# Performance work log

Hardware: AMD Instinct MI355X
Metric: run time of the kernel (lower is better)

Reference implementation:

```python
import jax, jax.numpy as jnp
import numpy as np

B, K, C, D, L, H, FF = 64, 1024, 512, 256, 2, 4, 1024
DH = D // H
EPS = 1e-5
NEG = -jnp.inf
SCALE = 1.0 / float(np.sqrt(DH))


def _ln(x, w, b):
    m = x.mean(-1, keepdims=True)
    v = ((x - m) ** 2).mean(-1, keepdims=True)
    return (x - m) * jax.lax.rsqrt(v + EPS) * w + b


def _star_attn(x, key_pad, pad_c, Wq, bq, Wk, bk, Wv, bv, Wo, bo):
    # Star topology: rows 0,1 (query,dustbin) attend to all non-padded keys;
    # each candidate row attends only to {query, dustbin, itself}.
    Bb, S, _ = x.shape
    q = (x @ Wq.T + bq).reshape(Bb, S, H, DH)
    k = (x @ Wk.T + bk).reshape(Bb, S, H, DH)
    v = (x @ Wv.T + bv).reshape(Bb, S, H, DH)
    # global rows
    qg = q[:, :2]
    sg = jnp.einsum('bthd,bshd->bhts', qg, k) * SCALE            # [B,H,2,S]
    sg = jnp.where(key_pad[:, None, None, :], NEG, sg)
    out_g = jnp.einsum('bhts,bshd->bthd', jax.nn.softmax(sg, -1), v)  # [B,2,H,DH]
    # candidate rows: scores against the 2 global keys + self key
    qc, kc, vc = q[:, 2:], k[:, 2:], v[:, 2:]
    kg, vg = k[:, :2], v[:, :2]
    s2 = jnp.einsum('bkhd,bthd->bkht', qc, kg) * SCALE           # [B,K,H,2]
    ss = jnp.einsum('bkhd,bkhd->bkh', qc, kc) * SCALE            # [B,K,H]
    ss = jnp.where(pad_c[:, :, None], NEG, ss)                   # padded self-key disallowed
    w = jax.nn.softmax(jnp.concatenate([s2, ss[..., None]], -1), -1)  # [B,K,H,3]
    out_c = jnp.einsum('bkht,bthd->bkhd', w[..., :2], vg) + w[..., 2:] * vc
    out = jnp.concatenate([out_g, out_c], 1).reshape(Bb, S, D)
    return out @ Wo.T + bo


def _forward(query, candidates, candidate_mask, qp_w, qp_b, cp_w, cp_b,
             dustbin, type_emb, ln1_w, ln1_b, ln2_w, ln2_b,
             Wq, bq, Wk, bk, Wv, bv, Wo, bo,
             ff1_w, ff1_b, ff2_w, ff2_b, head_ln_w, head_ln_b, head_w, head_b):
    Bb = query.shape[0]
    qt = (query @ qp_w.T + qp_b + type_emb[0])[:, None]          # [B,1,D]
    dt = jnp.broadcast_to(dustbin + type_emb[1], (Bb, 1, D))
    ct = candidates @ cp_w.T + cp_b + type_emb[2]                # [B,K,D]
    x = jnp.concatenate([qt, dt, ct], 1)                         # [B,K+2,D]
    pad_c = jnp.logical_not(candidate_mask)
    key_pad = jnp.concatenate([jnp.zeros((Bb, 2), bool), pad_c], 1)
    for l in range(L):  # pre-LN encoder layers (norm_first, eval so dropout=0)
        x = x + _star_attn(_ln(x, ln1_w[l], ln1_b[l]), key_pad, pad_c,
                           Wq[l], bq[l], Wk[l], bk[l], Wv[l], bv[l], Wo[l], bo[l])
        h = _ln(x, ln2_w[l], ln2_b[l])
        x = x + (jax.nn.gelu(h @ ff1_w[l].T + ff1_b[l], approximate=False) @ ff2_w[l].T + ff2_b[l])
    logits = (_ln(x, head_ln_w, head_ln_b) @ head_w.T + head_b)[..., 0]  # [B,K+2]
    cand = jnp.where(candidate_mask, logits[:, 2:], NEG)
    return jnp.concatenate([logits[:, 1:2], cand], 1)            # [B,K+1]


def setup_inputs() -> dict:
    key = jax.random.key(0)
    ks = iter(jax.random.split(key, 40))
    n = lambda shape, s=0.02: jax.random.normal(next(ks), shape, jnp.float32) * s
    return dict(
        query=jax.random.normal(next(ks), (B, C), jnp.float32),
        candidates=jax.random.normal(next(ks), (B, K, C), jnp.float32),
        candidate_mask=jax.random.bernoulli(next(ks), 0.9, (B, K)),
        qp_w=n((D, C)), qp_b=jnp.zeros(D),
        cp_w=n((D, C)), cp_b=jnp.zeros(D),
        dustbin=n((D,)), type_emb=n((3, D)),
        ln1_w=jnp.ones((L, D)), ln1_b=jnp.zeros((L, D)),
        ln2_w=jnp.ones((L, D)), ln2_b=jnp.zeros((L, D)),
        Wq=n((L, D, D)), bq=jnp.zeros((L, D)),
        Wk=n((L, D, D)), bk=jnp.zeros((L, D)),
        Wv=n((L, D, D)), bv=jnp.zeros((L, D)),
        Wo=n((L, D, D)), bo=jnp.zeros((L, D)),
        ff1_w=n((L, FF, D)), ff1_b=jnp.zeros((L, FF)),
        ff2_w=n((L, D, FF)), ff2_b=jnp.zeros((L, D)),
        head_ln_w=jnp.ones(D), head_ln_b=jnp.zeros(D),
        head_w=n((1, D)), head_b=jnp.zeros(1),
    )


def reference(query, candidates, candidate_mask, qp_w, qp_b, cp_w, cp_b,
              dustbin, type_emb, ln1_w, ln1_b, ln2_w, ln2_b,
              Wq, bq, Wk, bk, Wv, bv, Wo, bo,
              ff1_w, ff1_b, ff2_w, ff2_b, head_ln_w, head_ln_b, head_w, head_b):
    return _forward(query, candidates, candidate_mask, qp_w, qp_b, cp_w, cp_b,
                    dustbin, type_emb, ln1_w, ln1_b, ln2_w, ln2_b,
                    Wq, bq, Wk, bk, Wv, bv, Wo, bo,
                    ff1_w, ff1_b, ff2_w, ff2_b, head_ln_w, head_ln_b, head_w, head_b)
```

## Files before the change

kernel.cpp:

```cpp
#include <hip/hip_runtime.h>
#include <math.h>

static constexpr int Bc = 64;
static constexpr int Kc = 1024;
static constexpr int Cc = 512;
static constexpr int Dc = 256;
static constexpr int Hc = 4;
static constexpr int Sc = 1026;
static constexpr int FFc = 1024;
static constexpr float EPSc = 1e-5f;
static constexpr float SCALEc = 0.125f;
static constexpr float NEG_OUT = -1.0e30f;

typedef __attribute__((ext_vector_type(8))) short short8;
typedef __attribute__((ext_vector_type(8))) unsigned short u16x8;
typedef __attribute__((ext_vector_type(4))) float f32x4;

__device__ __forceinline__ float bf2f(unsigned short u) {
  union { float f; unsigned int i; } c; c.i = ((unsigned int)u) << 16; return c.f;
}
__device__ __forceinline__ unsigned short f2bf(float f) {
  union { float f; unsigned int i; } c; c.f = f;
  unsigned int i = c.i;
  unsigned int r = (i + 0x7fffu + ((i >> 16) & 1u)) >> 16;
  return (unsigned short)r;
}
__device__ __forceinline__ unsigned int cvt_pk_bf16(float a, float b) {
  unsigned int d;
  asm("v_cvt_pk_bf16_f32 %0, %1, %2" : "=v"(d) : "v"(a), "v"(b));
  return d;
}

__device__ __forceinline__ float wave_sum(float v) {
#pragma unroll
  for (int off = 32; off > 0; off >>= 1) v += __shfl_xor(v, off, 64);
  return v;
}
__device__ __forceinline__ float wave_max(float v) {
#pragma unroll
  for (int off = 32; off > 0; off >>= 1) v = fmaxf(v, __shfl_xor(v, off, 64));
  return v;
}

__device__ __forceinline__ void async_ld16(const unsigned short* g, unsigned short* l) {
  __builtin_amdgcn_global_load_lds(
      (const __attribute__((address_space(1))) void*)g,
      (__attribute__((address_space(3))) void*)l, 16, 0, 0);
}

__device__ __forceinline__ float gelu_fast(float u) {
  const float z = u * fmaf(u * u, 0.07135481627f, 1.5957691216f);
  return __fdividef(u, 1.0f + __expf(-z));
}

template <int EPI, int MAP, int CASTA>
__global__ __launch_bounds__(256) void gemm_mfma(
    const void* __restrict__ Av, const unsigned short* __restrict__ W,
    const float* __restrict__ bias, const void* extra,
    void* Cout, int N, int Kd, int ldc, int MB, int NB) {
  __shared__ unsigned short lds[24576];
  const int xcd = blockIdx.x & 7;
  const int slot = blockIdx.x >> 3;
  const int nb = slot % NB;
  const int mb = (slot / NB) * 8 + xcd;
  if (mb >= MB) return;
  const int m0 = mb * 128;
  const int n0 = nb * 128;
  const int tid = threadIdx.x;
  const int w = tid >> 6;
  const int lane = tid & 63;

  const unsigned short* A = (const unsigned short*)Av;
  const float* Af = (const float*)Av;

  const int srA[2] = {(w * 2 + 0) * 16 + (lane >> 2), (w * 2 + 1) * 16 + (lane >> 2)};
  const unsigned short* pA[2];
  const unsigned short* pB[2];
#pragma unroll
  for (int c = 0; c < 2; ++c) {
    const int kc = ((lane & 3) ^ ((srA[c] >> 1) & 3)) * 8;
    if (!CASTA) pA[c] = A + (size_t)(m0 + srA[c]) * Kd + kc;
    pB[c] = W + (size_t)(n0 + srA[c]) * Kd + kc;
  }
  const int lreg0 = (w * 2 + 0) * 512;
  const int lreg1 = (w * 2 + 1) * 512;

  f32x4 zero = {0.f, 0.f, 0.f, 0.f};
  f32x4 acc[4][4];
#pragma unroll
  for (int i = 0; i < 4; ++i)
#pragma unroll
    for (int j = 0; j < 4; ++j) acc[i][j] = zero;

  const int mrow = (w & 1) * 64;
  const int nrow = (w >> 1) * 64;
  const int l15 = lane & 15;
  const int quad = lane >> 4;
  const int koff = (quad ^ ((l15 >> 1) & 3)) * 16;

  auto stage = [&](int kk, int b) {
    if (CASTA) {
#pragma unroll
      for (int wi = 0; wi < 4; ++wi) {
        const int g = wi * 256 + tid;
        const int row = g >> 3;
        const int k4 = g & 7;
        const int phys =
            row * 32 + ((((k4 >> 1) ^ ((row >> 1) & 3))) << 3) + ((k4 & 1) << 2);
        const float4 a4 =
            *(const float4*)(Af + (size_t)(m0 + row) * Kd + kk + k4 * 4);
        uint2 o;
        o.x = cvt_pk_bf16(a4.x, a4.y);
        o.y = cvt_pk_bf16(a4.z, a4.w);
        *(uint2*)(&lds[b * 4096 + phys]) = o;
      }
    } else {
      async_ld16(pA[0] + kk, &lds[b * 4096 + lreg0]);
      async_ld16(pA[1] + kk, &lds[b * 4096 + lreg1]);
    }
    async_ld16(pB[0] + kk, &lds[12288 + b * 4096 + lreg0]);
    async_ld16(pB[1] + kk, &lds[12288 + b * 4096 + lreg1]);
  };

  auto compute_tile = [&](int cur) {
    const char* AsB = (const char*)&lds[cur * 4096];
    const char* WsB = (const char*)&lds[12288 + cur * 4096];
    short8 af[4], bfr[4];
#pragma unroll
    for (int i = 0; i < 4; ++i)
      af[i] = *(const short8*)(AsB + (size_t)(mrow + i * 16 + l15) * 64 + koff);
#pragma unroll
    for (int j = 0; j < 4; ++j)
      bfr[j] = *(const short8*)(WsB + (size_t)(nrow + j * 16 + l15) * 64 + koff);
#pragma unroll
    for (int i = 0; i < 4; ++i)
#pragma unroll
      for (int j = 0; j < 4; ++j)
        acc[i][j] = __builtin_amdgcn_mfma_f32_16x16x32_bf16(bfr[j], af[i],
                                                            acc[i][j], 0, 0, 0);
  };

  const int niter = Kd >> 5;
  if (CASTA) {
    stage(0, 0);
    for (int it = 0; it < niter; ++it) {
      const int cur = it & 1;
      __syncthreads();
      if (it + 1 < niter) stage((it + 1) << 5, cur ^ 1);
      compute_tile(cur);
    }
  } else {
    stage(0, 0);
    stage(32, 1);
    int cur = 0;
    for (int it = 0; it < niter; ++it) {
      if (it + 1 < niter)
        asm volatile("s_waitcnt vmcnt(4)" ::: "memory");
      else
        asm volatile("s_waitcnt vmcnt(0)" ::: "memory");
      asm volatile("s_waitcnt lgkmcnt(0)" ::: "memory");
      __builtin_amdgcn_s_barrier();
      if (it + 2 < niter) {
        int b2 = cur + 2; if (b2 >= 3) b2 -= 3;
        stage((it + 2) << 5, b2);
      }
      compute_tile(cur);
      cur = (cur == 2) ? 0 : cur + 1;
    }
  }

  const float* extraF = (const float*)extra;
  const unsigned short* extraB = (const unsigned short*)extra;
  float4 bj[4];
#pragma unroll
  for (int j = 0; j < 4; ++j) {
    const int n = n0 + nrow + j * 16 + quad * 4;
    float4 t4 = *(const float4*)(bias + n);
    if (EPI == 1) {
      const float4 e4 = *(const float4*)(extraF + n);
      t4.x += e4.x; t4.y += e4.y; t4.z += e4.z; t4.w += e4.w;
    }
    bj[j] = t4;
  }
  __syncthreads();
#pragma unroll
  for (int i = 0; i < 4; ++i) {
    const int m = mrow + i * 16 + l15;
    const int swz = (m & 7) << 1;
#pragma unroll
    for (int j = 0; j < 4; ++j) {
      float v0 = acc[i][j][0] + bj[j].x;
      float v1 = acc[i][j][1] + bj[j].y;
      float v2 = acc[i][j][2] + bj[j].z;
      float v3 = acc[i][j][3] + bj[j].w;
      if (EPI == 3) {
        v0 = gelu_fast(v0); v1 = gelu_fast(v1);
        v2 = gelu_fast(v2); v3 = gelu_fast(v3);
      }
      uint2 pk;
      pk.x = cvt_pk_bf16(v0, v1);
      pk.y = cvt_pk_bf16(v2, v3);
      const int g = ((nrow + j * 16 + quad * 4) >> 2) ^ swz;
      *(uint2*)(&lds[m * 128 + g * 4]) = pk;
    }
  }
  __syncthreads();
  unsigned short* outb = (unsigned short*)Cout;
#pragma unroll
  for (int c8 = 0; c8 < 8; ++c8) {
    const int idx = c8 * 256 + tid;
    const int row = idx >> 4;
    const int cc = idx & 15;
    const int gsr = (2 * cc) ^ ((row & 7) << 1);
    u16x8 val = *(const u16x8*)(&lds[row * 128 + gsr * 4]);
    const int col = cc * 8;
    const int m = m0 + row;
    const size_t orow =
        (MAP == 1) ? ((size_t)(m >> 10) * Sc + 2 + (m & 1023)) : (size_t)m;
    const size_t go = orow * (size_t)ldc + n0 + col;
    if (EPI == 2) {
      u16x8 rv = *(const u16x8*)(extraB + go);
      unsigned int* vp = (unsigned int*)&val;
#pragma unroll
      for (int e = 0; e < 4; ++e) {
        const float a0 = bf2f(val[2 * e]) + bf2f(rv[2 * e]);
        const float a1 = bf2f(val[2 * e + 1]) + bf2f(rv[2 * e + 1]);
        vp[e] = cvt_pk_bf16(a0, a1);
      }
    }
    *(u16x8*)(outb + go) = val;
  }
}

struct CastTab {
  const float* src[10];
  unsigned short* dst[10];
  int n4[10];
};
__global__ __launch_bounds__(256) void cast_multi(CastTab t) {
  const int e = blockIdx.y;
  const int n4 = t.n4[e];
  const float4* s = (const float4*)t.src[e];
  uint2* d = (uint2*)t.dst[e];
  for (int i = blockIdx.x * 256 + threadIdx.x; i < n4; i += gridDim.x * 256) {
    float4 f = s[i];
    uint2 o;
    o.x = cvt_pk_bf16(f.x, f.y);
    o.y = cvt_pk_bf16(f.z, f.w);
    d[i] = o;
  }
}

__global__ __launch_bounds__(256) void bias_concat(const float* bq, const float* bk,
                                                   const float* bv, float* qkvb) {
  const int i = blockIdx.x * 256 + threadIdx.x;
  if (i >= 2 * 768) return;
  const int l = i / 768;
  const int j = i - l * 768;
  float v;
  if (j < 256) v = bq[l * 256 + j];
  else if (j < 512) v = bk[l * 256 + j - 256];
  else v = bv[l * 256 + j - 512];
  qkvb[i] = v;
}

__global__ __launch_bounds__(256) void embed_qd(
    const float* __restrict__ qin, const float* __restrict__ qp_w,
    const float* __restrict__ qp_b, const float* __restrict__ dustbin,
    const float* __restrict__ type_emb, unsigned short* __restrict__ x) {
  const int b = blockIdx.x;
  const int d = threadIdx.x;
  __shared__ __align__(16) float qs[512];
  qs[d] = qin[b * 512 + d];
  qs[d + 256] = qin[b * 512 + 256 + d];
  __syncthreads();
  float acc = 0.0f;
  const float* wr = qp_w + (size_t)d * 512;
#pragma unroll 4
  for (int c = 0; c < 512; c += 4) {
    float4 w4 = *(const float4*)(wr + c);
    acc = fmaf(qs[c], w4.x, acc);
    acc = fmaf(qs[c + 1], w4.y, acc);
    acc = fmaf(qs[c + 2], w4.z, acc);
    acc = fmaf(qs[c + 3], w4.w, acc);
  }
  const size_t base = (size_t)b * Sc * Dc;
  x[base + d] = f2bf(acc + qp_b[d] + type_emb[d]);
  x[base + Dc + d] = f2bf(dustbin[d] + type_emb[Dc + d]);
}

__global__ __launch_bounds__(256) void ln_kernel(
    const unsigned short* __restrict__ x, const float* __restrict__ w,
    const float* __restrict__ b, unsigned short* __restrict__ y, int nrows) {
  const int wave = threadIdx.x >> 6;
  const int lane = threadIdx.x & 63;
  const int row = blockIdx.x * 4 + wave;
  if (row >= nrows) return;
  const unsigned short* xr = x + (size_t)row * Dc;
  ushort4 xv = *(const ushort4*)(xr + lane * 4);
  const float v0 = bf2f(xv.x), v1 = bf2f(xv.y), v2 = bf2f(xv.z), v3 = bf2f(xv.w);
  float s = v0 + v1 + v2 + v3;
  float sq = v0 * v0 + v1 * v1 + v2 * v2 + v3 * v3;
  s = wave_sum(s);
  sq = wave_sum(sq);
  const float mean = s * (1.0f / Dc);
  const float var = sq * (1.0f / Dc) - mean * mean;
  const float rs = rsqrtf(var + EPSc);
  float4 wv = *(const float4*)(w + lane * 4);
  float4 bv = *(const float4*)(b + lane * 4);
  uint2 o;
  o.x = cvt_pk_bf16((v0 - mean) * rs * wv.x + bv.x,
                    (v1 - mean) * rs * wv.y + bv.y);
  o.y = cvt_pk_bf16((v2 - mean) * rs * wv.z + bv.z,
                    (v3 - mean) * rs * wv.w + bv.w);
  *(uint2*)(y + (size_t)row * Dc + lane * 4) = o;
}

__global__ __launch_bounds__(256) void attn_global(
    const unsigned short* __restrict__ qkv, const unsigned char* __restrict__ mask,
    unsigned short* __restrict__ ao) {
  const int b = blockIdx.x;
  const int h = blockIdx.y;
  const int tid = threadIdx.x;
  const int wv = tid >> 6;
  const int lane = tid & 63;
  __shared__ float q0s[64], q1s[64];
  __shared__ float sc0[Sc], sc1[Sc];
  __shared__ float rbuf[4][2];
  __shared__ float obuf[2][4][64];
  const size_t base = (size_t)b * Sc * 768 + h * 64;
  if (tid < 64) {
    q0s[tid] = bf2f(qkv[base + tid]);
    q1s[tid] = bf2f(qkv[base + 768 + tid]);
  }
  __syncthreads();

  float lm0 = -INFINITY, lm1 = -INFINITY;
  for (int s = tid; s < Sc; s += 256) {
    const unsigned short* kr = qkv + base + 256 + (size_t)s * 768;
    float d0 = 0.0f, d1 = 0.0f;
#pragma unroll
    for (int c = 0; c < 64; c += 8) {
      u16x8 kv = *(const u16x8*)(kr + c);
#pragma unroll
      for (int e = 0; e < 8; ++e) {
        const float kf = bf2f(kv[e]);
        d0 = fmaf(q0s[c + e], kf, d0);
        d1 = fmaf(q1s[c + e], kf, d1);
      }
    }
    const bool pad = (s >= 2) && (mask[b * Kc + (s - 2)] == 0);
    const float s0 = pad ? -INFINITY : d0 * SCALEc;
    const float s1 = pad ? -INFINITY : d1 * SCALEc;
    sc0[s] = s0; sc1[s] = s1;
    lm0 = fmaxf(lm0, s0); lm1 = fmaxf(lm1, s1);
  }
  lm0 = wave_max(lm0);
  lm1 = wave_max(lm1);
  if (lane == 0) { rbuf[wv][0] = lm0; rbuf[wv][1] = lm1; }
  __syncthreads();
  const float m0 = fmaxf(fmaxf(rbuf[0][0], rbuf[1][0]), fmaxf(rbuf[2][0], rbuf[3][0]));
  const float m1 = fmaxf(fmaxf(rbuf[0][1], rbuf[1][1]), fmaxf(rbuf[2][1], rbuf[3][1]));
  float ls0 = 0.0f, ls1 = 0.0f;
  for (int s = tid; s < Sc; s += 256) {
    const float e0 = expf(sc0[s] - m0);
    const float e1 = expf(sc1[s] - m1);
    sc0[s] = e0; sc1[s] = e1;
    ls0 += e0; ls1 += e1;
  }
  ls0 = wave_sum(ls0);
  ls1 = wave_sum(ls1);
  __syncthreads();
  if (lane == 0) { rbuf[wv][0] = ls0; rbuf[wv][1] = ls1; }
  __syncthreads();
  const float t0 = rbuf[0][0] + rbuf[1][0] + rbuf[2][0] + rbuf[3][0];
  const float t1 = rbuf[0][1] + rbuf[1][1] + rbuf[2][1] + rbuf[3][1];
  float o0 = 0.0f, o1 = 0.0f;
  for (int s = wv; s < Sc; s += 4) {
    const float vvv = bf2f(qkv[base + 512 + (size_t)s * 768 + lane]);
    o0 = fmaf(sc0[s], vvv, o0);
    o1 = fmaf(sc1[s], vvv, o1);
  }
  obuf[0][wv][lane] = o0;
  obuf[1][wv][lane] = o1;
  __syncthreads();
  if (wv == 0) {
    const float a0 = obuf[0][0][lane] + obuf[0][1][lane] + obuf[0][2][lane] + obuf[0][3][lane];
    const float a1 = obuf[1][0][lane] + obuf[1][1][lane] + obuf[1][2][lane] + obuf[1][3][lane];
    const size_t ob = ((size_t)b * Sc) * Dc + h * 64;
    ao[ob + lane] = f2bf(a0 / t0);
    ao[ob + Dc + lane] = f2bf(a1 / t1);
  }
}

__global__ __launch_bounds__(256) void attn_cand(
    const unsigned short* __restrict__ qkv, const unsigned char* __restrict__ mask,
    unsigned short* __restrict__ ao) {
  const int bk = blockIdx.x;
  const int b = bk >> 10;
  const int kk = bk & 1023;
  const int h = threadIdx.x >> 6;
  const int lane = threadIdx.x & 63;
  const size_t rowg = (size_t)b * Sc * 768 + h * 64;
  const size_t rowc = rowg + (size_t)(2 + kk) * 768;
  const float qc = bf2f(qkv[rowc + lane]);
  float p0 = qc * bf2f(qkv[rowg + 256 + lane]);
  float p1 = qc * bf2f(qkv[rowg + 256 + 768 + lane]);
  float p2 = qc * bf2f(qkv[rowc + 256 + lane]);
#pragma unroll
  for (int off = 32; off > 0; off >>= 1) {
    p0 += __shfl_xor(p0, off, 64);
    p1 += __shfl_xor(p1, off, 64);
    p2 += __shfl_xor(p2, off, 64);
  }
  const bool pad = (mask[b * Kc + kk] == 0);
  const float s0 = p0 * SCALEc;
  const float s1 = p1 * SCALEc;
  const float s2 = pad ? -INFINITY : p2 * SCALEc;
  const float m = fmaxf(fmaxf(s0, s1), s2);
  const float e0 = expf(s0 - m);
  const float e1 = expf(s1 - m);
  const float e2 = pad ? 0.0f : expf(s2 - m);
  const float inv = 1.0f / (e0 + e1 + e2);
  const float o = (e0 * bf2f(qkv[rowg + 512 + lane]) +
                   e1 * bf2f(qkv[rowg + 512 + 768 + lane]) +
                   e2 * bf2f(qkv[rowc + 512 + lane])) * inv;
  ao[((size_t)b * Sc + 2 + kk) * Dc + h * 64 + lane] = f2bf(o);
}

__global__ __launch_bounds__(256) void head_kernel(
    const unsigned short* __restrict__ x, const float* __restrict__ lnw,
    const float* __restrict__ lnb, const float* __restrict__ hw,
    const float* __restrict__ hb, const unsigned char* __restrict__ mask,
    float* __restrict__ out) {
  const int gw = blockIdx.x * 4 + (threadIdx.x >> 6);
  const int lane = threadIdx.x & 63;
  if (gw >= Bc * 1025) return;
  const int b = gw / 1025;
  const int j = gw - b * 1025;
  const int s = 1 + j;
  const unsigned short* xr = x + ((size_t)b * Sc + s) * Dc;
  ushort4 xv = *(const ushort4*)(xr + lane * 4);
  const float v0 = bf2f(xv.x), v1 = bf2f(xv.y), v2 = bf2f(xv.z), v3 = bf2f(xv.w);
  float su = v0 + v1 + v2 + v3;
  float sq = v0 * v0 + v1 * v1 + v2 * v2 + v3 * v3;
  su = wave_sum(su);
  sq = wave_sum(sq);
  const float mean = su * (1.0f / Dc);
  const float var = sq * (1.0f / Dc) - mean * mean;
  const float rs = rsqrtf(var + EPSc);
  float4 wv = *(const float4*)(lnw + lane * 4);
  float4 bv = *(const float4*)(lnb + lane * 4);
  float4 hv = *(const float4*)(hw + lane * 4);
  float d = ((v0 - mean) * rs * wv.x + bv.x) * hv.x +
            ((v1 - mean) * rs * wv.y + bv.y) * hv.y +
            ((v2 - mean) * rs * wv.z + bv.z) * hv.z +
            ((v3 - mean) * rs * wv.w + bv.w) * hv.w;
  d = wave_sum(d);
  if (lane == 0) {
    const float logit = d + hb[0];
    float res;
    if (j == 0) res = logit;
    else res = (mask[b * Kc + (j - 1)] != 0) ? logit : NEG_OUT;
    out[(size_t)b * 1025 + j] = res;
  }
}

extern "C" void kernel_launch(void* const* d_in, const int* in_sizes, int n_in,
                              void* d_out, int out_size, void* d_ws,
                              size_t ws_size, hipStream_t stream) {
  const float* query = (const float*)d_in[0];
  const float* cands = (const float*)d_in[1];
  const unsigned char* mask = (const unsigned char*)d_in[2];
  const float* qp_w = (const float*)d_in[3];
  const float* qp_b = (const float*)d_in[4];
  const float* cp_w = (const float*)d_in[5];
  const float* cp_b = (const float*)d_in[6];
  const float* dustbin = (const float*)d_in[7];
  const float* type_emb = (const float*)d_in[8];
  const float* ln1_w = (const float*)d_in[9];
  const float* ln1_b = (const float*)d_in[10];
  const float* ln2_w = (const float*)d_in[11];
  const float* ln2_b = (const float*)d_in[12];
  const float* Wq = (const float*)d_in[13];
  const float* bq = (const float*)d_in[14];
  const float* Wk = (const float*)d_in[15];
  const float* bk = (const float*)d_in[16];
  const float* Wv = (const float*)d_in[17];
  const float* bv = (const float*)d_in[18];
  const float* Wo = (const float*)d_in[19];
  const float* bo = (const float*)d_in[20];
  const float* f1w = (const float*)d_in[21];
  const float* f1b = (const float*)d_in[22];
  const float* f2w = (const float*)d_in[23];
  const float* f2b = (const float*)d_in[24];
  const float* hlw = (const float*)d_in[25];
  const float* hlb = (const float*)d_in[26];
  const float* hw = (const float*)d_in[27];
  const float* hb = (const float*)d_in[28];
  float* out = (float*)d_out;

  const size_t XSZ = (size_t)Bc * Sc * Dc;
  const size_t FFSZ = (size_t)Bc * Sc * FFc;

  char* p = (char*)d_ws;
  unsigned short* x = (unsigned short*)p;   p += XSZ * 2;
  unsigned short* y = (unsigned short*)p;   p += XSZ * 2;
  unsigned short* ao = (unsigned short*)p;  p += XSZ * 2;
  unsigned short* big = (unsigned short*)p; p += FFSZ * 2;
  unsigned short* qkv = big;
  unsigned short* ff = big;
  unsigned short* cpw_b = (unsigned short*)p;
  unsigned short* qkvw_b = cpw_b + 131072;
  unsigned short* Wo_b = qkvw_b + 2 * 768 * 256;
  unsigned short* f1_b = Wo_b + 131072;
  unsigned short* f2_b = f1_b + 524288;
  float* qkvb = (float*)(f2_b + 524288);

  const int BS = Bc * Sc;
  auto sgrid = [](int MB, int NB) { return (unsigned)(NB * (((MB + 7) >> 3) << 3)); };

  CastTab t;
  t.src[0] = cp_w;  t.dst[0] = cpw_b; t.n4[0] = 131072 / 4;
  t.src[1] = Wo;    t.dst[1] = Wo_b;  t.n4[1] = 131072 / 4;
  t.src[2] = f1w;   t.dst[2] = f1_b;  t.n4[2] = 524288 / 4;
  t.src[3] = f2w;   t.dst[3] = f2_b;  t.n4[3] = 524288 / 4;
  for (int l = 0; l < 2; ++l) {
    t.src[4 + l * 3 + 0] = Wq + l * 65536;
    t.src[4 + l * 3 + 1] = Wk + l * 65536;
    t.src[4 + l * 3 + 2] = Wv + l * 65536;
    t.dst[4 + l * 3 + 0] = qkvw_b + l * 196608 + 0 * 65536;
    t.dst[4 + l * 3 + 1] = qkvw_b + l * 196608 + 1 * 65536;
    t.dst[4 + l * 3 + 2] = qkvw_b + l * 196608 + 2 * 65536;
    t.n4[4 + l * 3 + 0] = 65536 / 4;
    t.n4[4 + l * 3 + 1] = 65536 / 4;
    t.n4[4 + l * 3 + 2] = 65536 / 4;
  }
  cast_multi<<<dim3(128, 10), 256, 0, stream>>>(t);
  bias_concat<<<6, 256, 0, stream>>>(bq, bk, bv, qkvb);

  gemm_mfma<1, 1, 1><<<sgrid(512, 2), 256, 0, stream>>>(
      cands, cpw_b, cp_b, type_emb + 2 * Dc, x, Dc, Cc, Dc, 512, 2);
  embed_qd<<<Bc, 256, 0, stream>>>(query, qp_w, qp_b, dustbin, type_emb, x);

  for (int l = 0; l < 2; ++l) {
    ln_kernel<<<BS / 4, 256, 0, stream>>>(x, ln1_w + l * Dc, ln1_b + l * Dc, y, BS);
    gemm_mfma<4, 0, 0><<<sgrid(513, 6), 256, 0, stream>>>(
        y, qkvw_b + l * 196608, qkvb + l * 768, nullptr, qkv, 768, Dc, 768, 513, 6);
    attn_global<<<dim3(Bc, Hc), 256, 0, stream>>>(qkv, mask, ao);
    attn_cand<<<Bc * Kc, 256, 0, stream>>>(qkv, mask, ao);
    gemm_mfma<2, 0, 0><<<sgrid(513, 2), 256, 0, stream>>>(
        ao, Wo_b + l * 65536, bo + l * Dc, x, x, Dc, Dc, Dc, 513, 2);
    ln_kernel<<<BS / 4, 256, 0, stream>>>(x, ln2_w + l * Dc, ln2_b + l * Dc, y, BS);
    gemm_mfma<3, 0, 0><<<sgrid(513, 8), 256, 0, stream>>>(
        y, f1_b + l * 524288 / 2, f1b + l * FFc, nullptr, ff, FFc, Dc, FFc, 513, 8);
    gemm_mfma<2, 0, 0><<<sgrid(513, 2), 256, 0, stream>>>(
        ff, f2_b + l * 524288 / 2, f2b + l * Dc, x, x, Dc, FFc, Dc, 513, 2);
  }

  head_kernel<<<(Bc * 1025 + 3) / 4, 256, 0, stream>>>(x, hlw, hlb, hw, hb, mask, out);
}
```

Before: 999.4 us.

## Fuse FFN up and down projections into one kernel keeping hidden in LDS

Replaces the two FFN GEMM launches with a single kernel per 128-row tile. The kernel computes the FF1 output in 64-column chunks, applies GELU, stores the chunk in LDS and accumulates the FF2 product in registers, staging W1 and W2 chunks asynchronously. This removes the write and re-read of the large [B*S, 1024] hidden activation in global memory and one launch. In exchange it uses 513 blocks of 512 threads with 80KB LDS, which limits occupancy and recomputes nothing, but it serializes the chunk loop behind barriers.

```diff
diff --git a/kernel.cpp b/kernel.cpp
--- a/kernel.cpp
+++ b/kernel.cpp
@@ -52,6 +52,9 @@
   const float z = u * fmaf(u * u, 0.07135481627f, 1.5957691216f);
   return __fdividef(u, 1.0f + __expf(-z));
 }
+
+#define VMCNT0 asm volatile("s_waitcnt vmcnt(0)" ::: "memory")
+#define LGKM0  asm volatile("s_waitcnt lgkmcnt(0)" ::: "memory")
 
 template <int EPI, int MAP, int CASTA>
 __global__ __launch_bounds__(256) void gemm_mfma(
@@ -229,6 +232,185 @@
       }
     }
     *(u16x8*)(outb + go) = val;
+  }
+}
+
+__global__ __launch_bounds__(512, 2) void ff_fused2(
+    const unsigned short* __restrict__ Ay,
+    const unsigned short* __restrict__ W1,
+    const float* __restrict__ b1,
+    const unsigned short* __restrict__ W2,
+    const float* __restrict__ b2,
+    unsigned short* __restrict__ X) {
+  __shared__ __align__(16) char smem[81920];
+  char* sW1 = smem;
+  char* sW2 = smem + 32768;
+  char* sH  = smem + 65536;
+  const int m0 = blockIdx.x * 128;
+  const int tid = threadIdx.x;
+  const int w = tid >> 6;
+  const int lane = tid & 63;
+  const int l15 = lane & 15;
+  const int quad = lane >> 4;
+  const int wm = w >> 1;
+  const int wn = w & 1;
+  const int vm = w & 1;
+  const int vn = w >> 1;
+
+  auto stageW1 = [&](int c) {
+#pragma unroll
+    for (int k = 0; k < 4; ++k) {
+      const int o = k * 8192 + w * 1024 + lane * 16;
+      const int row = o >> 9;
+      const int g = ((o >> 4) & 31) ^ (row & 7);
+      async_ld16(W1 + (size_t)(c * 64 + row) * 256 + g * 8,
+                 (unsigned short*)(sW1 + k * 8192 + w * 1024));
+    }
+  };
+  auto stageW2 = [&](int c) {
+#pragma unroll
+    for (int k = 0; k < 4; ++k) {
+      const int o = k * 8192 + w * 1024 + lane * 16;
+      const int n = o >> 7;
+      const int g = ((o >> 4) & 7) ^ (n & 7);
+      async_ld16(W2 + (size_t)n * 1024 + c * 64 + g * 8,
+                 (unsigned short*)(sW2 + k * 8192 + w * 1024));
+    }
+  };
+
+  short8 areg[2][8];
+  {
+    const unsigned short* ap =
+        Ay + (size_t)(m0 + wm * 32 + l15) * 256 + quad * 8;
+#pragma unroll
+    for (int i = 0; i < 2; ++i)
+#pragma unroll
+      for (int ks = 0; ks < 8; ++ks)
+        areg[i][ks] = *(const short8*)(ap + i * 16 * 256 + ks * 32);
+  }
+
+  const f32x4 zero = {0.f, 0.f, 0.f, 0.f};
+  f32x4 acc2[4][4];
+#pragma unroll
+  for (int i = 0; i < 4; ++i)
+#pragma unroll
+    for (int j = 0; j < 4; ++j) acc2[i][j] = zero;
+
+  stageW1(0);
+
+  for (int c = 0; c < 16; ++c) {
+    VMCNT0;
+    LGKM0;
+    __builtin_amdgcn_s_barrier();
+    stageW2(c);
+
+    f32x4 acc1[2][2];
+#pragma unroll
+    for (int i = 0; i < 2; ++i)
+#pragma unroll
+      for (int j = 0; j < 2; ++j) acc1[i][j] = zero;
+#pragma unroll
+    for (int ks = 0; ks < 8; ++ks) {
+      short8 w1f[2];
+#pragma unroll
+      for (int j = 0; j < 2; ++j) {
+        const int r = wn * 32 + j * 16 + l15;
+        w1f[j] = *(const short8*)(sW1 + r * 512 +
+                                  (((ks * 4 + quad) ^ (r & 7)) << 4));
+      }
+#pragma unroll
+      for (int i = 0; i < 2; ++i)
+#pragma unroll
+        for (int j = 0; j < 2; ++j)
+          acc1[i][j] = __builtin_amdgcn_mfma_f32_16x16x32_bf16(
+              w1f[j], areg[i][ks], acc1[i][j], 0, 0, 0);
+    }
+    float4 bb[2];
+#pragma unroll
+    for (int j = 0; j < 2; ++j)
+      bb[j] = *(const float4*)(b1 + c * 64 + wn * 32 + j * 16 + quad * 4);
+#pragma unroll
+    for (int i = 0; i < 2; ++i) {
+      const int m = wm * 32 + i * 16 + l15;
+      const int swz = (m & 7) << 1;
+#pragma unroll
+      for (int j = 0; j < 2; ++j) {
+        const float v0 = gelu_fast(acc1[i][j][0] + bb[j].x);
+        const float v1 = gelu_fast(acc1[i][j][1] + bb[j].y);
+        const float v2 = gelu_fast(acc1[i][j][2] + bb[j].z);
+        const float v3 = gelu_fast(acc1[i][j][3] + bb[j].w);
+        uint2 pk;
+        pk.x = cvt_pk_bf16(v0, v1);
+        pk.y = cvt_pk_bf16(v2, v3);
+        const int g = ((wn * 32 + j * 16 + quad * 4) >> 2) ^ swz;
+        *(uint2*)(sH + m * 128 + g * 8) = pk;
+      }
+    }
+    LGKM0;
+    VMCNT0;
+    __builtin_amdgcn_s_barrier();
+    if (c + 1 < 16) stageW1(c + 1);
+
+#pragma unroll
+    for (int ks2 = 0; ks2 < 2; ++ks2) {
+      short8 hf[4], w2f[4];
+#pragma unroll
+      for (int i = 0; i < 4; ++i) {
+        const int hr = vm * 64 + i * 16 + l15;
+        const int g0 = (ks2 * 8 + quad * 2) ^ ((hr & 7) << 1);
+        hf[i] = *(const short8*)(sH + hr * 128 + g0 * 8);
+      }
+#pragma unroll
+      for (int j = 0; j < 4; ++j) {
+        const int r = vn * 64 + j * 16 + l15;
+        w2f[j] = *(const short8*)(sW2 + r * 128 +
+                                  (((ks2 * 4 + quad) ^ (r & 7)) << 4));
+      }
+#pragma unroll
+      for (int i = 0; i < 4; ++i)
+#pragma unroll
+        for (int j = 0; j < 4; ++j)
+          acc2[i][j] = __builtin_amdgcn_mfma_f32_16x16x32_bf16(
+              w2f[j], hf[i], acc2[i][j], 0, 0, 0);
+    }
+  }
+
+  LGKM0;
+  __builtin_amdgcn_s_barrier();
+#pragma unroll
+  for (int i = 0; i < 4; ++i) {
+    const int m = vm * 64 + i * 16 + l15;
+    const int swz = (m & 7) << 1;
+#pragma unroll
+    for (int j = 0; j < 4; ++j) {
+      const int n = vn * 64 + j * 16 + quad * 4;
+      const float4 b4 = *(const float4*)(b2 + n);
+      uint2 pk;
+      pk.x = cvt_pk_bf16(acc2[i][j][0] + b4.x, acc2[i][j][1] + b4.y);
+      pk.y = cvt_pk_bf16(acc2[i][j][2] + b4.z, acc2[i][j][3] + b4.w);
+      const int g = (n >> 2) ^ swz;
+      *(uint2*)(smem + m * 512 + g * 8) = pk;
+    }
+  }
+  LGKM0;
+  __builtin_amdgcn_s_barrier();
+#pragma unroll
+  for (int p = 0; p < 8; ++p) {
+    const int idx = p * 512 + tid;
+    const int row = idx >> 5;
+    const int s = idx & 31;
+    const int g0 = (s * 2) ^ ((row & 7) << 1);
+    u16x8 v = *(const u16x8*)(smem + row * 512 + g0 * 8);
+    unsigned short* xr = X + (size_t)(m0 + row) * 256 + s * 8;
+    u16x8 rv = *(const u16x8*)xr;
+    unsigned int* vp = (unsigned int*)&v;
+#pragma unroll
+    for (int e = 0; e < 4; ++e) {
+      const float a0 = bf2f(v[2 * e]) + bf2f(rv[2 * e]);
+      const float a1 = bf2f(v[2 * e + 1]) + bf2f(rv[2 * e + 1]);
+      vp[e] = cvt_pk_bf16(a0, a1);
+    }
+    *(u16x8*)xr = v;
   }
 }
 
@@ -509,7 +691,6 @@
   unsigned short* ao = (unsigned short*)p;  p += XSZ * 2;
   unsigned short* big = (unsigned short*)p; p += FFSZ * 2;
   unsigned short* qkv = big;
-  unsigned short* ff = big;
   unsigned short* cpw_b = (unsigned short*)p;
   unsigned short* qkvw_b = cpw_b + 131072;
   unsigned short* Wo_b = qkvw_b + 2 * 768 * 256;
@@ -552,10 +733,8 @@
     gemm_mfma<2, 0, 0><<<sgrid(513, 2), 256, 0, stream>>>(
         ao, Wo_b + l * 65536, bo + l * Dc, x, x, Dc, Dc, Dc, 513, 2);
     ln_kernel<<<BS / 4, 256, 0, stream>>>(x, ln2_w + l * Dc, ln2_b + l * Dc, y, BS);
-    gemm_mfma<3, 0, 0><<<sgrid(513, 8), 256, 0, stream>>>(
-        y, f1_b + l * 524288 / 2, f1b + l * FFc, nullptr, ff, FFc, Dc, FFc, 513, 8);
-    gemm_mfma<2, 0, 0><<<sgrid(513, 2), 256, 0, stream>>>(
-        ff, f2_b + l * 524288 / 2, f2b + l * Dc, x, x, Dc, FFc, Dc, 513, 2);
+    ff_fused2<<<513, 512, 0, stream>>>(
+        y, f1_b + l * 262144, f1b + l * FFc, f2_b + l * 262144, f2b + l * Dc, x);
   }
 
   head_kernel<<<(Bc * 1025 + 3) / 4, 256, 0, stream>>>(x, hlw, hlb, hw, hb, mask, out);
```

Result: slower. 1.047 ms (+4.8%).

## Widen MFMA GEMM output tile to 128x256 to halve A-tile re-reads

Applied to the files above, without the earlier changes.

The shared bf16 GEMM kernel now computes a 128x256 output tile per block instead of 128x128. Each wave holds a 64x128 accumulator block (4x8 MFMA tiles), and each stage issues four B loads per thread. The LDS staging buffers, the vmcnt wait threshold and the swizzled epilogue are resized to match, and every launch now uses half as many N-blocks. The aim is to halve how often activation tiles are re-read and to amortize A-fragment LDS reads over more MFMAs. In exchange it doubles accumulator registers and enlarges LDS, which can lower occupancy, and it halves the grid size, which can cause wave-quantization on the narrow D=256 GEMMs.

```diff
diff --git a/kernel.cpp b/kernel.cpp
--- a/kernel.cpp
+++ b/kernel.cpp
@@ -58,14 +58,14 @@
     const void* __restrict__ Av, const unsigned short* __restrict__ W,
     const float* __restrict__ bias, const void* extra,
     void* Cout, int N, int Kd, int ldc, int MB, int NB) {
-  __shared__ unsigned short lds[24576];
+  __shared__ unsigned short lds[36864];
   const int xcd = blockIdx.x & 7;
   const int slot = blockIdx.x >> 3;
   const int nb = slot % NB;
   const int mb = (slot / NB) * 8 + xcd;
   if (mb >= MB) return;
   const int m0 = mb * 128;
-  const int n0 = nb * 128;
+  const int n0 = nb * 256;
   const int tid = threadIdx.x;
   const int w = tid >> 6;
   const int lane = tid & 63;
@@ -73,27 +73,34 @@
   const unsigned short* A = (const unsigned short*)Av;
   const float* Af = (const float*)Av;
 
-  const int srA[2] = {(w * 2 + 0) * 16 + (lane >> 2), (w * 2 + 1) * 16 + (lane >> 2)};
+  const int rsub = lane >> 2;
   const unsigned short* pA[2];
-  const unsigned short* pB[2];
+  const unsigned short* pB[4];
 #pragma unroll
   for (int c = 0; c < 2; ++c) {
-    const int kc = ((lane & 3) ^ ((srA[c] >> 1) & 3)) * 8;
-    if (!CASTA) pA[c] = A + (size_t)(m0 + srA[c]) * Kd + kc;
-    pB[c] = W + (size_t)(n0 + srA[c]) * Kd + kc;
-  }
-  const int lreg0 = (w * 2 + 0) * 512;
-  const int lreg1 = (w * 2 + 1) * 512;
+    const int r = (w * 2 + c) * 16 + rsub;
+    const int kc = ((lane & 3) ^ ((r >> 1) & 3)) * 8;
+    if (!CASTA) pA[c] = A + (size_t)(m0 + r) * Kd + kc;
+  }
+#pragma unroll
+  for (int c = 0; c < 4; ++c) {
+    const int r = (w * 4 + c) * 16 + rsub;
+    const int kc = ((lane & 3) ^ ((r >> 1) & 3)) * 8;
+    pB[c] = W + (size_t)(n0 + r) * Kd + kc;
+  }
+  const int lregA[2] = {(w * 2 + 0) * 512, (w * 2 + 1) * 512};
+  const int lregB[4] = {(w * 4 + 0) * 512, (w * 4 + 1) * 512,
+                        (w * 4 + 2) * 512, (w * 4 + 3) * 512};
 
   f32x4 zero = {0.f, 0.f, 0.f, 0.f};
-  f32x4 acc[4][4];
+  f32x4 acc[4][8];
 #pragma unroll
   for (int i = 0; i < 4; ++i)
 #pragma unroll
-    for (int j = 0; j < 4; ++j) acc[i][j] = zero;
+    for (int j = 0; j < 8; ++j) acc[i][j] = zero;
 
   const int mrow = (w & 1) * 64;
-  const int nrow = (w >> 1) * 64;
+  const int ncol = (w >> 1) * 128;
   const int l15 = lane & 15;
   const int quad = lane >> 4;
   const int koff = (quad ^ ((l15 >> 1) & 3)) * 16;
@@ -115,27 +122,28 @@
         *(uint2*)(&lds[b * 4096 + phys]) = o;
       }
     } else {
-      async_ld16(pA[0] + kk, &lds[b * 4096 + lreg0]);
-      async_ld16(pA[1] + kk, &lds[b * 4096 + lreg1]);
-    }
-    async_ld16(pB[0] + kk, &lds[12288 + b * 4096 + lreg0]);
-    async_ld16(pB[1] + kk, &lds[12288 + b * 4096 + lreg1]);
+      async_ld16(pA[0] + kk, &lds[b * 4096 + lregA[0]]);
+      async_ld16(pA[1] + kk, &lds[b * 4096 + lregA[1]]);
+    }
+#pragma unroll
+    for (int c = 0; c < 4; ++c)
+      async_ld16(pB[c] + kk, &lds[12288 + b * 8192 + lregB[c]]);
   };
 
   auto compute_tile = [&](int cur) {
     const char* AsB = (const char*)&lds[cur * 4096];
-    const char* WsB = (const char*)&lds[12288 + cur * 4096];
-    short8 af[4], bfr[4];
+    const char* WsB = (const char*)&lds[12288 + cur * 8192];
+    short8 af[4], bfr[8];
 #pragma unroll
     for (int i = 0; i < 4; ++i)
       af[i] = *(const short8*)(AsB + (size_t)(mrow + i * 16 + l15) * 64 + koff);
 #pragma unroll
-    for (int j = 0; j < 4; ++j)
-      bfr[j] = *(const short8*)(WsB + (size_t)(nrow + j * 16 + l15) * 64 + koff);
+    for (int j = 0; j < 8; ++j)
+      bfr[j] = *(const short8*)(WsB + (size_t)(ncol + j * 16 + l15) * 64 + koff);
 #pragma unroll
     for (int i = 0; i < 4; ++i)
 #pragma unroll
-      for (int j = 0; j < 4; ++j)
+      for (int j = 0; j < 8; ++j)
         acc[i][j] = __builtin_amdgcn_mfma_f32_16x16x32_bf16(bfr[j], af[i],
                                                             acc[i][j], 0, 0, 0);
   };
@@ -155,7 +163,7 @@
     int cur = 0;
     for (int it = 0; it < niter; ++it) {
       if (it + 1 < niter)
-        asm volatile("s_waitcnt vmcnt(4)" ::: "memory");
+        asm volatile("s_waitcnt vmcnt(6)" ::: "memory");
       else
         asm volatile("s_waitcnt vmcnt(0)" ::: "memory");
       asm volatile("s_waitcnt lgkmcnt(0)" ::: "memory");
@@ -171,10 +179,10 @@
 
   const float* extraF = (const float*)extra;
   const unsigned short* extraB = (const unsigned short*)extra;
-  float4 bj[4];
-#pragma unroll
-  for (int j = 0; j < 4; ++j) {
-    const int n = n0 + nrow + j * 16 + quad * 4;
+  float4 bj[8];
+#pragma unroll
+  for (int j = 0; j < 8; ++j) {
+    const int n = n0 + ncol + j * 16 + quad * 4;
     float4 t4 = *(const float4*)(bias + n);
     if (EPI == 1) {
       const float4 e4 = *(const float4*)(extraF + n);
@@ -188,7 +196,7 @@
     const int m = mrow + i * 16 + l15;
     const int swz = (m & 7) << 1;
 #pragma unroll
-    for (int j = 0; j < 4; ++j) {
+    for (int j = 0; j < 8; ++j) {
       float v0 = acc[i][j][0] + bj[j].x;
       float v1 = acc[i][j][1] + bj[j].y;
       float v2 = acc[i][j][2] + bj[j].z;
@@ -200,20 +208,20 @@
       uint2 pk;
       pk.x = cvt_pk_bf16(v0, v1);
       pk.y = cvt_pk_bf16(v2, v3);
-      const int g = ((nrow + j * 16 + quad * 4) >> 2) ^ swz;
-      *(uint2*)(&lds[m * 128 + g * 4]) = pk;
+      const int g = ((ncol + j * 16 + quad * 4) >> 2) ^ swz;
+      *(uint2*)(&lds[m * 256 + g * 4]) = pk;
     }
   }
   __syncthreads();
   unsigned short* outb = (unsigned short*)Cout;
 #pragma unroll
-  for (int c8 = 0; c8 < 8; ++c8) {
-    const int idx = c8 * 256 + tid;
-    const int row = idx >> 4;
-    const int cc = idx & 15;
-    const int gsr = (2 * cc) ^ ((row & 7) << 1);
-    u16x8 val = *(const u16x8*)(&lds[row * 128 + gsr * 4]);
-    const int col = cc * 8;
+  for (int p = 0; p < 16; ++p) {
+    const int idx = p * 256 + tid;
+    const int row = idx >> 5;
+    const int s = idx & 31;
+    const int gsr = (2 * s) ^ ((row & 7) << 1);
+    u16x8 val = *(const u16x8*)(&lds[row * 256 + gsr * 4]);
+    const int col = s * 8;
     const int m = m0 + row;
     const size_t orow =
         (MAP == 1) ? ((size_t)(m >> 10) * Sc + 2 + (m & 1023)) : (size_t)m;
@@ -539,23 +547,23 @@
   cast_multi<<<dim3(128, 10), 256, 0, stream>>>(t);
   bias_concat<<<6, 256, 0, stream>>>(bq, bk, bv, qkvb);
 
-  gemm_mfma<1, 1, 1><<<sgrid(512, 2), 256, 0, stream>>>(
-      cands, cpw_b, cp_b, type_emb + 2 * Dc, x, Dc, Cc, Dc, 512, 2);
+  gemm_mfma<1, 1, 1><<<sgrid(512, 1), 256, 0, stream>>>(
+      cands, cpw_b, cp_b, type_emb + 2 * Dc, x, Dc, Cc, Dc, 512, 1);
   embed_qd<<<Bc, 256, 0, stream>>>(query, qp_w, qp_b, dustbin, type_emb, x);
 
   for (int l = 0; l < 2; ++l) {
     ln_kernel<<<BS / 4, 256, 0, stream>>>(x, ln1_w + l * Dc, ln1_b + l * Dc, y, BS);
-    gemm_mfma<4, 0, 0><<<sgrid(513, 6), 256, 0, stream>>>(
-        y, qkvw_b + l * 196608, qkvb + l * 768, nullptr, qkv, 768, Dc, 768, 513, 6);
+    gemm_mfma<4, 0, 0><<<sgrid(513, 3), 256, 0, stream>>>(
+        y, qkvw_b + l * 196608, qkvb + l * 768, nullptr, qkv, 768, Dc, 768, 513, 3);
     attn_global<<<dim3(Bc, Hc), 256, 0, stream>>>(qkv, mask, ao);
     attn_cand<<<Bc * Kc, 256, 0, stream>>>(qkv, mask, ao);
-    gemm_mfma<2, 0, 0><<<sgrid(513, 2), 256, 0, stream>>>(
-        ao, Wo_b + l * 65536, bo + l * Dc, x, x, Dc, Dc, Dc, 513, 2);
+    gemm_mfma<2, 0, 0><<<sgrid(513, 1), 256, 0, stream>>>(
+        ao, Wo_b + l * 65536, bo + l * Dc, x, x, Dc, Dc, Dc, 513, 1);
     ln_kernel<<<BS / 4, 256, 0, stream>>>(x, ln2_w + l * Dc, ln2_b + l * Dc, y, BS);
-    gemm_mfma<3, 0, 0><<<sgrid(513, 8), 256, 0, stream>>>(
-        y, f1_b + l * 524288 / 2, f1b + l * FFc, nullptr, ff, FFc, Dc, FFc, 513, 8);
-    gemm_mfma<2, 0, 0><<<sgrid(513, 2), 256, 0, stream>>>(
-        ff, f2_b + l * 524288 / 2, f2b + l * Dc, x, x, Dc, FFc, Dc, 513, 2);
+    gemm_mfma<3, 0, 0><<<sgrid(513, 4), 256, 0, stream>>>(
+        y, f1_b + l * 524288 / 2, f1b + l * FFc, nullptr, ff, FFc, Dc, FFc, 513, 4);
+    gemm_mfma<2, 0, 0><<<sgrid(513, 1), 256, 0, stream>>>(
+        ff, f2_b + l * 524288 / 2, f2b + l * Dc, x, x, Dc, FFc, Dc, 513, 1);
   }
 
   head_kernel<<<(Bc * 1025 + 3) / 4, 256, 0, stream>>>(x, hlw, hlb, hw, hb, mask, out);
```

Measured after the change: 1.190 ms. +19.1%, slower.
